# Kernel optimization log

Measured on AMD Instinct MI355X. Metric: run time of the kernel, lower is better.

## Reference

```python
import jax, jax.numpy as jnp
import numpy as np

HEADS = 8
DIM_HEAD = 64
SCALE = DIM_HEAD ** -0.5


def setup_inputs() -> dict:
    key = jax.random.key(0)
    ks = jax.random.split(key, 6)
    B, N, D = 4, 2048, 512
    inner = HEADS * DIM_HEAD  # 512
    x = jax.random.normal(ks[0], (B, N, D), dtype=jnp.float32)
    centroid_delta = jax.random.normal(ks[1], (B, 3, N, N), dtype=jnp.float32)
    Wqkv = jax.random.normal(ks[2], (D, 3 * inner), dtype=jnp.float32) * (D ** -0.5)
    Wout = jax.random.normal(ks[3], (inner, D), dtype=jnp.float32) * (inner ** -0.5)
    bout = jnp.zeros((D,), dtype=jnp.float32)
    rel_w = jax.random.normal(ks[4], (HEADS, 3), dtype=jnp.float32)
    rel_b = jnp.zeros((HEADS,), dtype=jnp.float32)
    return {"x": x, "centroid_delta": centroid_delta, "Wqkv": Wqkv,
            "Wout": Wout, "bout": bout, "rel_w": rel_w, "rel_b": rel_b}


def reference(x, centroid_delta, Wqkv, Wout, bout, rel_w, rel_b):
    B, N, D = x.shape
    h, d = HEADS, DIM_HEAD
    qkv = x @ Wqkv                      # [B, N, 3*h*d]
    q, k, v = jnp.split(qkv, 3, axis=-1)
    # [B, N, h*d] -> [B, h, N, d]
    reshape = lambda t: t.reshape(B, N, h, d).transpose(0, 2, 1, 3)
    q, k, v = reshape(q), reshape(k), reshape(v)
    dots = jnp.einsum('bhid,bhjd->bhij', q, k) * SCALE  # [B, h, N, N]
    # 1x1 conv: Conv2d(3, heads, 1) on centroid_delta [B, 3, N, N]
    bias = jnp.einsum('hc,bcij->bhij', rel_w, centroid_delta) + rel_b[None, :, None, None]
    attn = jax.nn.softmax(dots + bias, axis=-1)
    out = jnp.einsum('bhij,bhjd->bhid', attn, v)        # [B, h, N, d]
    out = out.transpose(0, 2, 1, 3).reshape(B, N, h * d)
    return out @ Wout + bout
```

## Files before the change

### kernel.cpp

```cpp
#include <hip/hip_runtime.h>
#include <hip/hip_bf16.h>

typedef __bf16 bf16_t;
typedef __bf16 bf16x8 __attribute__((ext_vector_type(8)));
typedef float f32x4 __attribute__((ext_vector_type(4)));

#define SCALE_ 0.125f
#define BATCH 4
#define NSEQ 2048
#define DMODEL 512
#define HEADS 8
#define DHEAD 64
#define QKVN 1536
#define NN ((size_t)NSEQ * NSEQ)

#define BAR() asm volatile("s_waitcnt lgkmcnt(0)\n\ts_barrier" ::: "memory")

__device__ __forceinline__ void gload_lds16(const void* g, void* l) {
  __builtin_amdgcn_global_load_lds((const __attribute__((address_space(1))) void*)g,
                                   (__attribute__((address_space(3))) void*)l, 16, 0, 0);
}

__device__ __forceinline__ f32x4 mfma16(bf16x8 a, bf16x8 b, f32x4 c) {
  return __builtin_amdgcn_mfma_f32_16x16x32_bf16(a, b, c, 0, 0, 0);
}

__global__ __launch_bounds__(256) void cvt_bf16_kernel(const float* __restrict__ in,
                                                       bf16_t* __restrict__ out, int n4) {
  int i = blockIdx.x * 256 + threadIdx.x;
  if (i < n4) {
    float4 v = ((const float4*)in)[i];
    union { bf16_t b[4]; uint2 u; } pk;
    pk.b[0] = (bf16_t)v.x; pk.b[1] = (bf16_t)v.y;
    pk.b[2] = (bf16_t)v.z; pk.b[3] = (bf16_t)v.w;
    ((uint2*)out)[i] = pk.u;
  }
}

__global__ __launch_bounds__(256) void cvt_transpose_kernel(const float* __restrict__ in,
                                                            bf16_t* __restrict__ out, int R, int C) {
  __shared__ float tile[64][65];
  const int r0 = blockIdx.y * 64, c0 = blockIdx.x * 64;
  const int tx = threadIdx.x & 63, tg = threadIdx.x >> 6;
#pragma unroll
  for (int i = 0; i < 16; i++) {
    int rr = tg * 16 + i;
    tile[rr][tx] = in[(size_t)(r0 + rr) * C + c0 + tx];
  }
  __syncthreads();
#pragma unroll
  for (int i = 0; i < 16; i++) {
    int cc = tg * 16 + i;
    out[(size_t)(c0 + cc) * R + r0 + tx] = (bf16_t)tile[tx][cc];
  }
}

template<int BIAS, int OUTF32>
__global__ __launch_bounds__(256) void gemm128_kernel(const bf16_t* __restrict__ A,
    const bf16_t* __restrict__ Bt, void* __restrict__ Cout,
    const float* __restrict__ bias, int M, int N, int K) {
  __shared__ __align__(16) bf16_t As[128 * 64];
  __shared__ __align__(16) bf16_t Bs[128 * 64];
  const int tid = threadIdx.x;
  const int w = tid >> 6, lane = tid & 63, quad = lane >> 4, l16 = lane & 15;
  const int wm = w & 1, wn = w >> 1;
  const int m0 = blockIdx.x * 128, n0 = blockIdx.y * 128;
  f32x4 acc[4][4] = {};
  int srow[4], scg[4];
#pragma unroll
  for (int t = 0; t < 4; t++) {
    int s = (w * 4 + t) * 64 + lane;
    srow[t] = s >> 3;
    scg[t] = (s & 7) ^ (srow[t] & 7);
  }
  for (int k0 = 0; k0 < K; k0 += 64) {
#pragma unroll
    for (int t = 0; t < 4; t++) {
      gload_lds16(&A[(size_t)(m0 + srow[t]) * K + k0 + scg[t] * 8], &As[(w * 4 + t) * 512]);
      gload_lds16(&Bt[(size_t)(n0 + srow[t]) * K + k0 + scg[t] * 8], &Bs[(w * 4 + t) * 512]);
    }
    __syncthreads();
    bf16x8 af[4][2], bfr[4][2];
#pragma unroll
    for (int mt = 0; mt < 4; mt++) {
      int row = wm * 64 + mt * 16 + l16;
#pragma unroll
      for (int kh = 0; kh < 2; kh++)
        af[mt][kh] = *(const bf16x8*)&As[(row * 8 + ((kh * 4 + quad) ^ (row & 7))) * 8];
    }
#pragma unroll
    for (int nt = 0; nt < 4; nt++) {
      int row = wn * 64 + nt * 16 + l16;
#pragma unroll
      for (int kh = 0; kh < 2; kh++)
        bfr[nt][kh] = *(const bf16x8*)&Bs[(row * 8 + ((kh * 4 + quad) ^ (row & 7))) * 8];
    }
#pragma unroll
    for (int mt = 0; mt < 4; mt++)
#pragma unroll
      for (int nt = 0; nt < 4; nt++) {
        acc[mt][nt] = mfma16(af[mt][0], bfr[nt][0], acc[mt][nt]);
        acc[mt][nt] = mfma16(af[mt][1], bfr[nt][1], acc[mt][nt]);
      }
    __syncthreads();
  }
#pragma unroll
  for (int nt = 0; nt < 4; nt++) {
    int col = n0 + wn * 64 + nt * 16 + l16;
    float bv = BIAS ? bias[col] : 0.0f;
#pragma unroll
    for (int mt = 0; mt < 4; mt++) {
#pragma unroll
      for (int rr = 0; rr < 4; rr++) {
        int row = m0 + wm * 64 + mt * 16 + quad * 4 + rr;
        float v = acc[mt][nt][rr] + bv;
        if (OUTF32) ((float*)Cout)[(size_t)row * N + col] = v;
        else        ((bf16_t*)Cout)[(size_t)row * N + col] = (bf16_t)v;
      }
    }
  }
}

__global__ __launch_bounds__(256, 4) void attn_kernel(const bf16_t* __restrict__ qkv,
    const float* __restrict__ cd, const float* __restrict__ rel_w,
    const float* __restrict__ rel_b, bf16_t* __restrict__ ao) {
  __shared__ __align__(16) bf16_t Ks[64][72];
  __shared__ __align__(16) bf16_t Vts[64][72];
  __shared__ __align__(16) bf16_t Ps[64][72];
  const int tid = threadIdx.x;
  const int w = tid >> 6, lane = tid & 63, quad = lane >> 4, l16 = lane & 15;
  const int bid = blockIdx.x;
  const int h = bid >> 7, b = (bid >> 5) & 3, it = bid & 31;

  const size_t qoff = (size_t)(b * NSEQ + it * 64 + w * 16 + l16) * QKVN + h * DHEAD;
  bf16x8 q0 = *(const bf16x8*)&qkv[qoff + quad * 8];
  bf16x8 q1 = *(const bf16x8*)&qkv[qoff + 32 + quad * 8];

  const float rw0 = rel_w[h * 3 + 0], rw1 = rel_w[h * 3 + 1], rw2 = rel_w[h * 3 + 2];
  const float rb = rel_b[h];

  f32x4 o[4] = {};
  float m_r[4], l_r[4];
#pragma unroll
  for (int r = 0; r < 4; r++) { m_r[r] = -1e30f; l_r[r] = 0.0f; }

  const int sr = tid >> 3, sg = tid & 7;
  const size_t kbase = (size_t)b * NSEQ * QKVN + DMODEL + h * DHEAD;

  const int row0 = it * 64 + w * 16 + quad * 4;
  const float* cdp = cd + (size_t)b * 3 * NN + (size_t)row0 * NSEQ + l16;
  float biasr[4][4];
#define LOADBIAS(JT) do { const int jb_ = (JT) * 64;                                   \
  _Pragma("unroll") for (int ct_ = 0; ct_ < 4; ct_++)                                  \
  _Pragma("unroll") for (int r_ = 0; r_ < 4; r_++) {                                   \
    size_t ci_ = (size_t)r_ * NSEQ + jb_ + ct_ * 16;                                   \
    biasr[ct_][r_] = fmaf(rw0, cdp[ci_],                                               \
                     fmaf(rw1, cdp[ci_ + NN], fmaf(rw2, cdp[ci_ + 2 * NN], rb)));      \
  } } while (0)

  uint4 k0r, k1r, v0r, v1r;
  {
    const bf16_t* p = &qkv[kbase + (size_t)sr * QKVN + sg * 8];
    k0r = *(const uint4*)p;               v0r = *(const uint4*)(p + DMODEL);
    k1r = *(const uint4*)(p + 32 * QKVN); v1r = *(const uint4*)(p + 32 * QKVN + DMODEL);
  }
  LOADBIAS(0);

  for (int jt = 0; jt < 32; jt++) {
    *(uint4*)&Ks[sr][sg * 8]      = k0r;
    *(uint4*)&Ks[sr + 32][sg * 8] = k1r;
    {
      union { bf16_t e[8]; uint4 u; } va, vb; va.u = v0r; vb.u = v1r;
      const int pc = sr ^ ((sg & 3) << 3);
#pragma unroll
      for (int e2 = 0; e2 < 8; e2++) {
        Vts[sg * 8 + e2][pc]      = va.e[e2];
        Vts[sg * 8 + e2][pc + 32] = vb.e[e2];
      }
    }
    BAR();

    if (jt < 31) {
      const bf16_t* p = &qkv[kbase + (size_t)((jt + 1) * 64 + sr) * QKVN + sg * 8];
      k0r = *(const uint4*)p;               v0r = *(const uint4*)(p + DMODEL);
      k1r = *(const uint4*)(p + 32 * QKVN); v1r = *(const uint4*)(p + 32 * QKVN + DMODEL);
    }

    f32x4 s[4] = {};
#pragma unroll
    for (int ct = 0; ct < 4; ct++) {
      bf16x8 b0 = *(const bf16x8*)&Ks[ct * 16 + l16][quad * 8];
      bf16x8 b1 = *(const bf16x8*)&Ks[ct * 16 + l16][32 + quad * 8];
      s[ct] = mfma16(q0, b0, s[ct]);
      s[ct] = mfma16(q1, b1, s[ct]);
    }

#pragma unroll
    for (int ct = 0; ct < 4; ct++)
#pragma unroll
      for (int r = 0; r < 4; r++)
        s[ct][r] = s[ct][r] * SCALE_ + biasr[ct][r];
    if (jt < 31) LOADBIAS(jt + 1);

#pragma unroll
    for (int r = 0; r < 4; r++) {
      float mx = fmaxf(fmaxf(s[0][r], s[1][r]), fmaxf(s[2][r], s[3][r]));
#pragma unroll
      for (int off = 8; off >= 1; off >>= 1) mx = fmaxf(mx, __shfl_xor(mx, off, 64));
      float mnew = fmaxf(m_r[r], mx);
      float alpha = __expf(m_r[r] - mnew);
      float rsum = 0.0f;
#pragma unroll
      for (int ct = 0; ct < 4; ct++) {
        float p = __expf(s[ct][r] - mnew);
        s[ct][r] = p; rsum += p;
      }
#pragma unroll
      for (int off = 8; off >= 1; off >>= 1) rsum += __shfl_xor(rsum, off, 64);
      l_r[r] = l_r[r] * alpha + rsum;
      m_r[r] = mnew;
#pragma unroll
      for (int dt = 0; dt < 4; dt++) o[dt][r] *= alpha;
    }

#pragma unroll
    for (int ct = 0; ct < 4; ct++)
#pragma unroll
      for (int rr = 0; rr < 4; rr++)
        Ps[w * 16 + quad * 4 + rr][(ct * 16 + l16) ^ (quad << 3)] = (bf16_t)s[ct][rr];

    const int psw = ((l16 >> 2) & 3) << 3;
    bf16x8 p0 = *(const bf16x8*)&Ps[w * 16 + l16][(quad * 8) ^ psw];
    bf16x8 p1 = *(const bf16x8*)&Ps[w * 16 + l16][32 + ((quad * 8) ^ psw)];
#pragma unroll
    for (int dt = 0; dt < 4; dt++) {
      const int row = dt * 16 + l16;
      const int vsw = ((row >> 3) & 3) << 3;
      bf16x8 v0 = *(const bf16x8*)&Vts[row][(quad * 8) ^ vsw];
      bf16x8 v1 = *(const bf16x8*)&Vts[row][32 + ((quad * 8) ^ vsw)];
      o[dt] = mfma16(p0, v0, o[dt]);
      o[dt] = mfma16(p1, v1, o[dt]);
    }
    BAR();
  }

#pragma unroll
  for (int dt = 0; dt < 4; dt++) {
    int col = h * DHEAD + dt * 16 + l16;
#pragma unroll
    for (int rr = 0; rr < 4; rr++) {
      int row = b * NSEQ + it * 64 + w * 16 + quad * 4 + rr;
      ao[(size_t)row * DMODEL + col] = (bf16_t)(o[dt][rr] / l_r[rr]);
    }
  }
#undef LOADBIAS
}

extern "C" void kernel_launch(void* const* d_in, const int* in_sizes, int n_in,
                              void* d_out, int out_size, void* d_ws, size_t ws_size,
                              hipStream_t stream) {
  const float* x     = (const float*)d_in[0];
  const float* cd    = (const float*)d_in[1];
  const float* Wqkv  = (const float*)d_in[2];
  const float* Wout  = (const float*)d_in[3];
  const float* bout  = (const float*)d_in[4];
  const float* rel_w = (const float*)d_in[5];
  const float* rel_b = (const float*)d_in[6];
  float* out = (float*)d_out;

  char* ws = (char*)d_ws;
  const size_t M = (size_t)BATCH * NSEQ;
  bf16_t* xb    = (bf16_t*)ws;
  bf16_t* WqkvT = (bf16_t*)(ws + 8388608);
  bf16_t* WoutT = (bf16_t*)(ws + 8388608 + 1572864);
  bf16_t* qkv   = (bf16_t*)(ws + 8388608 + 1572864 + 524288);
  bf16_t* ao    = (bf16_t*)(ws + 8388608 + 1572864 + 524288 + 25165824);

  cvt_bf16_kernel<<<(int)(M * DMODEL / 4 / 256), 256, 0, stream>>>(x, xb, (int)(M * DMODEL / 4));
  cvt_transpose_kernel<<<dim3(QKVN / 64, DMODEL / 64), 256, 0, stream>>>(Wqkv, WqkvT, DMODEL, QKVN);
  cvt_transpose_kernel<<<dim3(DMODEL / 64, DMODEL / 64), 256, 0, stream>>>(Wout, WoutT, DMODEL, DMODEL);

  gemm128_kernel<0, 0><<<dim3(M / 128, QKVN / 128), 256, 0, stream>>>(
      xb, WqkvT, (void*)qkv, nullptr, (int)M, QKVN, DMODEL);

  attn_kernel<<<BATCH * 32 * HEADS, 256, 0, stream>>>(qkv, cd, rel_w, rel_b, ao);

  gemm128_kernel<1, 1><<<dim3(M / 128, DMODEL / 128), 256, 0, stream>>>(
      ao, WoutT, (void*)out, bout, (int)M, DMODEL, DMODEL);
}
```

Measured before the change: 447.0 us.

## Transpose QK^T MFMA so each lane owns one query row for softmax

Swaps the MFMA operand order so the score tile is transposed: each lane holds four consecutive key columns of a single query row. The centroid_delta bias can then be read with 16-byte vector loads along rows instead of scalar strided loads, and the row max/sum reductions need two cross-lane shuffles instead of four per row. Alpha and l are redistributed to the output layout with __shfl, P is written to LDS as packed 8-byte stores, and the final division becomes a reciprocal multiply. This trades extra shuffles for remapping against fewer bias load instructions and less reduction work.

```diff
diff --git a/kernel.cpp b/kernel.cpp
--- a/kernel.cpp
+++ b/kernel.cpp
@@ -140,22 +140,21 @@
   const float rb = rel_b[h];
 
   f32x4 o[4] = {};
-  float m_r[4], l_r[4];
-#pragma unroll
-  for (int r = 0; r < 4; r++) { m_r[r] = -1e30f; l_r[r] = 0.0f; }
+  float m_r = -1e30f, l_r = 0.0f;
 
   const int sr = tid >> 3, sg = tid & 7;
   const size_t kbase = (size_t)b * NSEQ * QKVN + DMODEL + h * DHEAD;
 
-  const int row0 = it * 64 + w * 16 + quad * 4;
-  const float* cdp = cd + (size_t)b * 3 * NN + (size_t)row0 * NSEQ + l16;
-  float biasr[4][4];
-#define LOADBIAS(JT) do { const int jb_ = (JT) * 64;                                   \
-  _Pragma("unroll") for (int ct_ = 0; ct_ < 4; ct_++)                                  \
-  _Pragma("unroll") for (int r_ = 0; r_ < 4; r_++) {                                   \
-    size_t ci_ = (size_t)r_ * NSEQ + jb_ + ct_ * 16;                                   \
-    biasr[ct_][r_] = fmaf(rw0, cdp[ci_],                                               \
-                     fmaf(rw1, cdp[ci_ + NN], fmaf(rw2, cdp[ci_ + 2 * NN], rb)));      \
+  const int qrow = it * 64 + w * 16 + l16;
+  const float* cdp = cd + (size_t)b * 3 * NN + (size_t)qrow * NSEQ + quad * 4;
+  f32x4 biasr[4];
+#define LOADBIAS(JT) do { const size_t jb_ = (size_t)(JT) * 64;                        \
+  _Pragma("unroll") for (int ct_ = 0; ct_ < 4; ct_++) {                                \
+    f32x4 c0_ = *(const f32x4*)(cdp + jb_ + ct_ * 16);                                 \
+    f32x4 c1_ = *(const f32x4*)(cdp + NN + jb_ + ct_ * 16);                            \
+    f32x4 c2_ = *(const f32x4*)(cdp + 2 * NN + jb_ + ct_ * 16);                        \
+    _Pragma("unroll") for (int r_ = 0; r_ < 4; r_++)                                   \
+      biasr[ct_][r_] = fmaf(rw0, c0_[r_], fmaf(rw1, c1_[r_], fmaf(rw2, c2_[r_], rb))); \
   } } while (0)
 
   uint4 k0r, k1r, v0r, v1r;
@@ -189,10 +188,10 @@
     f32x4 s[4] = {};
 #pragma unroll
     for (int ct = 0; ct < 4; ct++) {
-      bf16x8 b0 = *(const bf16x8*)&Ks[ct * 16 + l16][quad * 8];
-      bf16x8 b1 = *(const bf16x8*)&Ks[ct * 16 + l16][32 + quad * 8];
-      s[ct] = mfma16(q0, b0, s[ct]);
-      s[ct] = mfma16(q1, b1, s[ct]);
+      bf16x8 kf0 = *(const bf16x8*)&Ks[ct * 16 + l16][quad * 8];
+      bf16x8 kf1 = *(const bf16x8*)&Ks[ct * 16 + l16][32 + quad * 8];
+      s[ct] = mfma16(kf0, q0, s[ct]);
+      s[ct] = mfma16(kf1, q1, s[ct]);
     }
 
 #pragma unroll
@@ -202,36 +201,51 @@
         s[ct][r] = s[ct][r] * SCALE_ + biasr[ct][r];
     if (jt < 31) LOADBIAS(jt + 1);
 
+    float mx;
+    {
+      float a0 = fmaxf(fmaxf(s[0][0], s[0][1]), fmaxf(s[0][2], s[0][3]));
+      float a1 = fmaxf(fmaxf(s[1][0], s[1][1]), fmaxf(s[1][2], s[1][3]));
+      float a2 = fmaxf(fmaxf(s[2][0], s[2][1]), fmaxf(s[2][2], s[2][3]));
+      float a3 = fmaxf(fmaxf(s[3][0], s[3][1]), fmaxf(s[3][2], s[3][3]));
+      mx = fmaxf(fmaxf(a0, a1), fmaxf(a2, a3));
+    }
+    mx = fmaxf(mx, __shfl_xor(mx, 16, 64));
+    mx = fmaxf(mx, __shfl_xor(mx, 32, 64));
+    const float mnew = fmaxf(m_r, mx);
+    const float alpha = __expf(m_r - mnew);
+    m_r = mnew;
+    float ts[4];
+#pragma unroll
+    for (int ct = 0; ct < 4; ct++) {
+      float p0_ = __expf(s[ct][0] - mnew);
+      float p1_ = __expf(s[ct][1] - mnew);
+      float p2_ = __expf(s[ct][2] - mnew);
+      float p3_ = __expf(s[ct][3] - mnew);
+      s[ct][0] = p0_; s[ct][1] = p1_; s[ct][2] = p2_; s[ct][3] = p3_;
+      ts[ct] = (p0_ + p1_) + (p2_ + p3_);
+    }
+    float rsum = (ts[0] + ts[1]) + (ts[2] + ts[3]);
+    rsum += __shfl_xor(rsum, 16, 64);
+    rsum += __shfl_xor(rsum, 32, 64);
+    l_r = l_r * alpha + rsum;
 #pragma unroll
     for (int r = 0; r < 4; r++) {
-      float mx = fmaxf(fmaxf(s[0][r], s[1][r]), fmaxf(s[2][r], s[3][r]));
-#pragma unroll
-      for (int off = 8; off >= 1; off >>= 1) mx = fmaxf(mx, __shfl_xor(mx, off, 64));
-      float mnew = fmaxf(m_r[r], mx);
-      float alpha = __expf(m_r[r] - mnew);
-      float rsum = 0.0f;
-#pragma unroll
-      for (int ct = 0; ct < 4; ct++) {
-        float p = __expf(s[ct][r] - mnew);
-        s[ct][r] = p; rsum += p;
-      }
-#pragma unroll
-      for (int off = 8; off >= 1; off >>= 1) rsum += __shfl_xor(rsum, off, 64);
-      l_r[r] = l_r[r] * alpha + rsum;
-      m_r[r] = mnew;
-#pragma unroll
-      for (int dt = 0; dt < 4; dt++) o[dt][r] *= alpha;
-    }
-
-#pragma unroll
-    for (int ct = 0; ct < 4; ct++)
-#pragma unroll
-      for (int rr = 0; rr < 4; rr++)
-        Ps[w * 16 + quad * 4 + rr][(ct * 16 + l16) ^ (quad << 3)] = (bf16_t)s[ct][rr];
-
-    const int psw = ((l16 >> 2) & 3) << 3;
-    bf16x8 p0 = *(const bf16x8*)&Ps[w * 16 + l16][(quad * 8) ^ psw];
-    bf16x8 p1 = *(const bf16x8*)&Ps[w * 16 + l16][32 + ((quad * 8) ^ psw)];
+      float aq = __shfl(alpha, quad * 20 + r, 64);
+#pragma unroll
+      for (int dt = 0; dt < 4; dt++) o[dt][r] *= aq;
+    }
+
+    const int prow = w * 16 + l16;
+    const int ksw = (l16 >> 2) & 3;
+#pragma unroll
+    for (int ct = 0; ct < 4; ct++) {
+      union { bf16_t e[4]; uint2 u; } pk;
+#pragma unroll
+      for (int r = 0; r < 4; r++) pk.e[r] = (bf16_t)s[ct][r];
+      *(uint2*)&Ps[prow][(ct * 16 + quad * 4) ^ (ksw << 3)] = pk.u;
+    }
+    bf16x8 p0 = *(const bf16x8*)&Ps[prow][(quad * 8) ^ (ksw << 3)];
+    bf16x8 p1 = *(const bf16x8*)&Ps[prow][(32 + quad * 8) ^ (ksw << 3)];
 #pragma unroll
     for (int dt = 0; dt < 4; dt++) {
       const int row = dt * 16 + l16;
@@ -244,13 +258,18 @@
     BAR();
   }
 
+  float lq[4];
+#pragma unroll
+  for (int rr = 0; rr < 4; rr++) lq[rr] = __shfl(l_r, quad * 20 + rr, 64);
+#pragma unroll
+  for (int rr = 0; rr < 4; rr++) lq[rr] = 1.0f / lq[rr];
 #pragma unroll
   for (int dt = 0; dt < 4; dt++) {
     int col = h * DHEAD + dt * 16 + l16;
 #pragma unroll
     for (int rr = 0; rr < 4; rr++) {
       int row = b * NSEQ + it * 64 + w * 16 + quad * 4 + rr;
-      ao[(size_t)row * DMODEL + col] = (bf16_t)(o[dt][rr] / l_r[rr]);
+      ao[(size_t)row * DMODEL + col] = (bf16_t)(o[dt][rr] * lq[rr]);
     }
   }
 #undef LOADBIAS
```

Measured after the change: 507.0 us. 1.13x slower.

## Pack row-max shuffles into fp16 pairs and compute softmax row sums via MFMA

Applied to the files above, without the earlier changes.

Replaces the per-row fp32 max shuffle reductions with packed fp16 max reductions, handling two rows per shuffle, which halves the cross-lane shuffle count for the max. It also drops the rsum shuffle reduction and gets the row sums by multiplying the bf16 P tile by a ones vector on the matrix cores. The fp16 max is only an approximation of the row max, but softmax is invariant to the exact offset, so this only risks overflow or precision loss for extreme values. Computing the sums from bf16-rounded P also makes them consistent with what feeds the PV product.

```diff
diff --git a/kernel.cpp b/kernel.cpp
--- a/kernel.cpp
+++ b/kernel.cpp
@@ -1,5 +1,6 @@
 #include <hip/hip_runtime.h>
 #include <hip/hip_bf16.h>
+#include <hip/hip_fp16.h>
 
 typedef __bf16 bf16_t;
 typedef __bf16 bf16x8 __attribute__((ext_vector_type(8)));
@@ -23,6 +24,12 @@
 
 __device__ __forceinline__ f32x4 mfma16(bf16x8 a, bf16x8 b, f32x4 c) {
   return __builtin_amdgcn_mfma_f32_16x16x32_bf16(a, b, c, 0, 0, 0);
+}
+
+__device__ __forceinline__ int pkmax_f16(int a, int b) {
+  int d;
+  asm("v_pk_max_f16 %0, %1, %2" : "=v"(d) : "v"(a), "v"(b));
+  return d;
 }
 
 __global__ __launch_bounds__(256) void cvt_bf16_kernel(const float* __restrict__ in,
@@ -139,6 +146,10 @@
   const float rw0 = rel_w[h * 3 + 0], rw1 = rel_w[h * 3 + 1], rw2 = rel_w[h * 3 + 2];
   const float rb = rel_b[h];
 
+  bf16x8 ones;
+#pragma unroll
+  for (int e = 0; e < 8; e++) ones[e] = (bf16_t)1.0f;
+
   f32x4 o[4] = {};
   float m_r[4], l_r[4];
 #pragma unroll
@@ -202,25 +213,33 @@
         s[ct][r] = s[ct][r] * SCALE_ + biasr[ct][r];
     if (jt < 31) LOADBIAS(jt + 1);
 
+    float mx[4];
+#pragma unroll
+    for (int r = 0; r < 4; r++)
+      mx[r] = fmaxf(fmaxf(s[0][r], s[1][r]), fmaxf(s[2][r], s[3][r]));
+    {
+      union { __half h[2]; int i; } u01, u23;
+      u01.h[0] = __float2half(mx[0]); u01.h[1] = __float2half(mx[1]);
+      u23.h[0] = __float2half(mx[2]); u23.h[1] = __float2half(mx[3]);
+#pragma unroll
+      for (int off = 8; off >= 1; off >>= 1) {
+        u01.i = pkmax_f16(u01.i, __shfl_xor(u01.i, off, 64));
+        u23.i = pkmax_f16(u23.i, __shfl_xor(u23.i, off, 64));
+      }
+      mx[0] = __half2float(u01.h[0]); mx[1] = __half2float(u01.h[1]);
+      mx[2] = __half2float(u23.h[0]); mx[3] = __half2float(u23.h[1]);
+    }
+    float alpha[4];
 #pragma unroll
     for (int r = 0; r < 4; r++) {
-      float mx = fmaxf(fmaxf(s[0][r], s[1][r]), fmaxf(s[2][r], s[3][r]));
-#pragma unroll
-      for (int off = 8; off >= 1; off >>= 1) mx = fmaxf(mx, __shfl_xor(mx, off, 64));
-      float mnew = fmaxf(m_r[r], mx);
-      float alpha = __expf(m_r[r] - mnew);
-      float rsum = 0.0f;
-#pragma unroll
-      for (int ct = 0; ct < 4; ct++) {
-        float p = __expf(s[ct][r] - mnew);
-        s[ct][r] = p; rsum += p;
-      }
-#pragma unroll
-      for (int off = 8; off >= 1; off >>= 1) rsum += __shfl_xor(rsum, off, 64);
-      l_r[r] = l_r[r] * alpha + rsum;
+      float mnew = fmaxf(m_r[r], mx[r]);
+      alpha[r] = __expf(m_r[r] - mnew);
       m_r[r] = mnew;
 #pragma unroll
-      for (int dt = 0; dt < 4; dt++) o[dt][r] *= alpha;
+      for (int ct = 0; ct < 4; ct++)
+        s[ct][r] = __expf(s[ct][r] - mnew);
+#pragma unroll
+      for (int dt = 0; dt < 4; dt++) o[dt][r] *= alpha[r];
     }
 
 #pragma unroll
@@ -240,6 +259,13 @@
       bf16x8 v1 = *(const bf16x8*)&Vts[row][32 + ((quad * 8) ^ vsw)];
       o[dt] = mfma16(p0, v0, o[dt]);
       o[dt] = mfma16(p1, v1, o[dt]);
+    }
+    {
+      f32x4 ls = {};
+      ls = mfma16(p0, ones, ls);
+      ls = mfma16(p1, ones, ls);
+#pragma unroll
+      for (int r = 0; r < 4; r++) l_r[r] = l_r[r] * alpha[r] + ls[r];
     }
     BAR();
   }
```

Result: no change. 441.6 us (median of 2 runs) (-1.2%).
